# Kernel tuning notes

Measured on AMD Instinct MI355X. Metric: run time of the kernel, lower is better.

## Reference

```python
import jax, jax.numpy as jnp
import numpy as np
import math

B, K, T = 4, 1024, 2048
OD, H = 128, 8


def setup_inputs() -> dict:
    key = jax.random.key(0)
    ks = jax.random.split(key, 6)
    s_in = 1.0 / math.sqrt(K)
    s_u = 1.0 / math.sqrt(H * OD)
    return {
        "x": jax.random.normal(ks[0], (B, K, T), dtype=jnp.float32),
        "Wk": jax.random.uniform(ks[1], (H * OD, K), minval=-s_in, maxval=s_in, dtype=jnp.float32),
        "Wq": jax.random.uniform(ks[2], (H * OD, K), minval=-s_in, maxval=s_in, dtype=jnp.float32),
        "Wv": jax.random.uniform(ks[3], (H * OD, K), minval=-s_in, maxval=s_in, dtype=jnp.float32),
        "Wu": jax.random.uniform(ks[4], (OD, H * OD), minval=-s_u, maxval=s_u, dtype=jnp.float32),
        "bu": jax.random.uniform(ks[5], (OD,), minval=-s_u, maxval=s_u, dtype=jnp.float32),
    }


def reference(x, Wk, Wq, Wv, Wu, bu):
    b, k, t = x.shape
    # QKV projections: Linear applied over channel dim of channels-first input
    keys = jnp.einsum('bkt,jk->bjt', x, Wk).reshape(b, H, OD, t)
    queries = jnp.einsum('bkt,jk->bjt', x, Wq).reshape(b, H, OD, t)
    values = jnp.einsum('bkt,jk->bjt', x, Wv).reshape(b, H, OD, t)
    # attention scores over time: [b, h, t, t]
    dot = jnp.einsum('bhkt,bhki->bhti', queries, keys) / math.sqrt(OD)
    dot = jax.nn.softmax(dot, axis=-1)
    out = jnp.einsum('bhti,bhki->bhkt', dot, values)  # [b, h, od, t]
    # unify heads: weight (OD, H*OD) viewed as (OD_out=k, H=h, OD=e)
    out = jnp.einsum('bhet,khe->bkt', out, Wu.reshape(OD, H, OD))
    return out + bu[None, :, None]
```

## Files before the change

kernel.cpp:

```cpp
#include <hip/hip_runtime.h>
#include <hip/hip_bf16.h>
#include <type_traits>
#include <utility>

#define DEVINL __device__ __forceinline__

typedef unsigned short u16;
typedef unsigned int   u32;
typedef short  s8v  __attribute__((ext_vector_type(8)));
typedef __bf16 b8v  __attribute__((ext_vector_type(8)));
typedef float  f4v  __attribute__((ext_vector_type(4)));
typedef float  f16v __attribute__((ext_vector_type(16)));
typedef u32    u4v  __attribute__((ext_vector_type(4)));

static constexpr int BB = 4, KD = 1024, TT = 2048, OD = 128, NH = 8;
static constexpr int J2 = 2048;

template<class V, class = void> struct mfma_takes : std::false_type {};
template<class V> struct mfma_takes<V, std::void_t<decltype(
    __builtin_amdgcn_mfma_f32_16x16x32_bf16(std::declval<V>(), std::declval<V>(),
                                            std::declval<f4v>(), 0, 0, 0))>> : std::true_type {};

template<class AV>
DEVINL f4v mfma16(AV a, AV b, f4v c) {
  if constexpr (mfma_takes<AV>::value) {
    return __builtin_amdgcn_mfma_f32_16x16x32_bf16(a, b, c, 0, 0, 0);
  } else {
    return __builtin_amdgcn_mfma_f32_16x16x32_bf16(
        __builtin_bit_cast(b8v, a), __builtin_bit_cast(b8v, b), c, 0, 0, 0);
  }
}

template<class V, class = void> struct mfma32_takes : std::false_type {};
template<class V> struct mfma32_takes<V, std::void_t<decltype(
    __builtin_amdgcn_mfma_f32_32x32x16_bf16(std::declval<V>(), std::declval<V>(),
                                            std::declval<f16v>(), 0, 0, 0))>> : std::true_type {};

template<class AV>
DEVINL f16v mfma32(AV a, AV b, f16v c) {
  if constexpr (mfma32_takes<AV>::value) {
    return __builtin_amdgcn_mfma_f32_32x32x16_bf16(a, b, c, 0, 0, 0);
  } else {
    return __builtin_amdgcn_mfma_f32_32x32x16_bf16(
        __builtin_bit_cast(b8v, a), __builtin_bit_cast(b8v, b), c, 0, 0, 0);
  }
}

DEVINL u16 f2bf(float f) {
  union { float f; u32 u; } v; v.f = f;
  u32 u = v.u;
  return (u16)((u + 0x7fffu + ((u >> 16) & 1u)) >> 16);
}
DEVINL float bf2f(u16 h) { union { u32 u; float f; } v; v.u = ((u32)h) << 16; return v.f; }

DEVINL u32 cvtpk_bf16(float a, float b) {
  u32 r;
  asm("v_cvt_pk_bf16_f32 %0, %1, %2" : "=v"(r) : "v"(a), "v"(b));
  return r;
}

DEVINL void gload_lds16(const void* g, void* l) {
  __builtin_amdgcn_global_load_lds(
      (const __attribute__((address_space(1))) void*)g,
      (__attribute__((address_space(3))) void*)l, 16, 0, 0);
}

__global__ void xpose_split_x(const float* __restrict__ x, u16* __restrict__ xTh) {
  __shared__ float tile[32][33];
  const int b  = blockIdx.z;
  const int k0 = blockIdx.y * 32;
  const int t0 = blockIdx.x * 32;
  const int tx = threadIdx.x;
  const int ty = threadIdx.y;
  const float* xb = x + (size_t)b * KD * TT;
#pragma unroll
  for (int j = 0; j < 4; ++j)
    tile[ty + j * 8][tx] = xb[(size_t)(k0 + ty + j * 8) * TT + t0 + tx];
  __syncthreads();
  u16* oh = xTh + (size_t)b * TT * KD;
#pragma unroll
  for (int j = 0; j < 4; ++j) {
    int t = ty + j * 8;
    float v = tile[tx][t];
    oh[(size_t)(t0 + t) * KD + k0 + tx] = f2bf(v);
  }
}

__global__ void split_weights(const float* __restrict__ Wk, const float* __restrict__ Wq,
                              const float* __restrict__ Wv, const float* __restrict__ Wu,
                              u16* __restrict__ Wkqh, u16* __restrict__ Wvh,
                              u16* __restrict__ Wuh,  u16* __restrict__ Wul,
                              float qscale) {
  int i = blockIdx.x * 256 + threadIdx.x;
  if (i < 1048576) {
    Wkqh[i] = f2bf(Wk[i]);
    Wkqh[1048576 + i] = f2bf(Wq[i] * qscale);
    Wvh[i] = f2bf(Wv[i]);
    if (i < 131072) {
      float v = Wu[i];  u16 hh = f2bf(v);
      Wuh[i] = hh;      Wul[i] = f2bf(v - bf2f(hh));
    }
  }
}

template<int EPI>
__global__ __launch_bounds__(256, 3) void gemm_bt_split(
    const u16* __restrict__ Ahi, const u16* __restrict__ Alo,
    const u16* __restrict__ Bhi, const u16* __restrict__ Blo,
    void* __restrict__ Couth,
    const float* __restrict__ bias,
    int Kdim, int ldc, long strideA, long strideB, long strideC, int npass) {
  __shared__ __align__(16) u16 At[128 * 64];
  __shared__ __align__(16) u16 Bt[128 * 64];
  const int tid = threadIdx.x;
  const int w = tid >> 6, l = tid & 63;
  const int wm = w >> 1, wn = w & 1;
  const int lr = l & 15, lg = l >> 4;
  const int b = blockIdx.z;
  const u16* Ah = Ahi + (size_t)b * strideA;
  const u16* Al = Alo ? Alo + (size_t)b * strideA : nullptr;
  const u16* Bh = Bhi + (size_t)b * strideB;
  const u16* Bl = Blo ? Blo + (size_t)b * strideB : nullptr;
  const int m0 = blockIdx.x * 128;
  const int n0 = (EPI == 3) ? ((blockIdx.y & 15) * 128) : (blockIdx.y * 128);
  const int ky = (EPI == 3) ? (blockIdx.y >> 4) : 0;
  const int kspan = (EPI == 3) ? (Kdim / 2) : Kdim;
  const int kbase = ky * kspan;

  int srow[4], soff[4];
#pragma unroll
  for (int i = 0; i < 4; ++i) {
    int c = tid + i * 256;
    int row = c >> 3, q = c & 7;
    srow[i] = row;
    soff[i] = (q ^ (row & 7)) * 8;
  }

  f4v acc[4][4] = {};

  const int spi = kspan / 64;
  const int iters = npass * spi;
  for (int it = 0; it < iters; ++it) {
    const int seg = it / spi;
    const int k = kbase + (it - seg * spi) * 64;
    const u16* As = (seg == 2) ? Al : Ah;
    const u16* Bs = (seg == 1) ? Bl : Bh;
#pragma unroll
    for (int i = 0; i < 4; ++i) {
      int c = tid + i * 256;
      gload_lds16(As + (size_t)(m0 + srow[i]) * Kdim + k + soff[i], (char*)At + c * 16);
      gload_lds16(Bs + (size_t)(n0 + srow[i]) * Kdim + k + soff[i], (char*)Bt + c * 16);
    }
    __syncthreads();
    __builtin_amdgcn_s_setprio(1);
#pragma unroll
    for (int kk = 0; kk < 2; ++kk) {
      const int q = kk * 4 + lg;
      s8v a[4], bb[4];
#pragma unroll
      for (int mi = 0; mi < 4; ++mi) {
        int row = wm * 64 + mi * 16 + lr;
        a[mi] = *(const s8v*)(&At[row * 64 + (q ^ (row & 7)) * 8]);
      }
#pragma unroll
      for (int ni = 0; ni < 4; ++ni) {
        int row = wn * 64 + ni * 16 + lr;
        bb[ni] = *(const s8v*)(&Bt[row * 64 + (q ^ (row & 7)) * 8]);
      }
#pragma unroll
      for (int mi = 0; mi < 4; ++mi)
#pragma unroll
        for (int ni = 0; ni < 4; ++ni)
          acc[mi][ni] = mfma16(a[mi], bb[ni], acc[mi][ni]);
    }
    __builtin_amdgcn_s_setprio(0);
    __syncthreads();
  }

  if constexpr (EPI == 2) {
    u16* Ch = (u16*)Couth + (size_t)b * strideC;
#pragma unroll
    for (int mi = 0; mi < 4; ++mi)
#pragma unroll
      for (int ni = 0; ni < 4; ++ni)
#pragma unroll
        for (int r = 0; r < 4; ++r) {
          int m = m0 + wm * 64 + mi * 16 + lg * 4 + r;
          int n = n0 + wn * 64 + ni * 16 + lr;
          Ch[(size_t)m * ldc + n] = f2bf(acc[mi][ni][r]);
        }
  } else if constexpr (EPI == 3) {
    float* C = (float*)Couth + ((size_t)ky * BB + b) * strideC;
#pragma unroll
    for (int mi = 0; mi < 4; ++mi)
#pragma unroll
      for (int ni = 0; ni < 4; ++ni)
#pragma unroll
        for (int r = 0; r < 4; ++r) {
          int m = m0 + wm * 64 + mi * 16 + lg * 4 + r;
          int n = n0 + wn * 64 + ni * 16 + lr;
          C[(size_t)m * ldc + n] = acc[mi][ni][r];
        }
  } else {
    float* C = (float*)Couth + (size_t)b * strideC;
#pragma unroll
    for (int mi = 0; mi < 4; ++mi)
#pragma unroll
      for (int ni = 0; ni < 4; ++ni)
#pragma unroll
        for (int r = 0; r < 4; ++r) {
          int m = m0 + wm * 64 + mi * 16 + lg * 4 + r;
          int n = n0 + wn * 64 + ni * 16 + lr;
          C[(size_t)m * ldc + n] = acc[mi][ni][r] + bias[m];
        }
  }
}

__global__ void addbias(const float* __restrict__ part, float* __restrict__ out,
                        const float* __restrict__ bias) {
  int i = blockIdx.x * 256 + threadIdx.x;
  f4v a = ((const f4v*)part)[i];
  f4v c = ((const f4v*)part)[i + 262144];
  float bs = bias[(i >> 9) & 127];
  f4v r;
#pragma unroll
  for (int j = 0; j < 4; ++j) r[j] = a[j] + c[j] + bs;
  ((f4v*)out)[i] = r;
}

__global__ __launch_bounds__(256, 3) void attn_fwd(
    const u16* __restrict__ QKTh, const u16* __restrict__ Vh,
    u16* __restrict__ OTh, u16* __restrict__ OTl) {
  __shared__ __align__(16) u16 Ksh[2][32 * 128];
  __shared__ __align__(16) u16 Vsh[2][128 * 32];

  const int bid = blockIdx.x;
  const int lid = (bid & 7) * 64 + (bid >> 3);
  const int t0 = (lid & 15) * 128;
  const int h  = (lid >> 4) & 7;
  const int b  = lid >> 7;

  const int tid = threadIdx.x;
  const int w = tid >> 6, l = tid & 63;
  const int lw = l & 31, hi = l >> 5;
  const size_t qb = (size_t)b * TT * J2;
  const u16* Qh_ = QKTh + qb + 1024 + h * 128;
  const u16* Kh_ = QKTh + qb + h * 128;
  const u16* Vh_ = Vh + (size_t)b * 1024 * TT + (size_t)h * 128 * TT;

  int koff[2], kdo[2], voff[2], vdo[2];
#pragma unroll
  for (int i = 0; i < 2; ++i) {
    int c = tid + i * 256;
    { int row = c >> 4, q = c & 15;
      koff[i] = row * J2 + (q ^ (row & 7)) * 8;  kdo[i] = c * 16; }
    { int row = c >> 2, q = c & 3;
      voff[i] = row * TT + (q ^ ((row >> 1) & 3)) * 8;  vdo[i] = c * 16; }
  }

#define ATTN_STAGE(BSEL, I0) do {                                          \
    _Pragma("unroll")                                                      \
    for (int i_ = 0; i_ < 2; ++i_) {                                       \
      gload_lds16(Kh_ + (size_t)(I0) * J2 + koff[i_], (char*)Ksh[BSEL] + kdo[i_]); \
      gload_lds16(Vh_ + voff[i_] + (I0),              (char*)Vsh[BSEL] + vdo[i_]); \
    } } while (0)

  s8v qh[8];
  {
    const size_t trow = (size_t)(t0 + w * 32 + lw) * J2;
#pragma unroll
    for (int st = 0; st < 8; ++st)
      qh[st] = *(const s8v*)(Qh_ + trow + st * 16 + hi * 8);
  }

  f16v o[4] = {};
  float mrow = -1e30f, lsum = 0.f;

  ATTN_STAGE(0, 0);

  for (int it = 0; it < 64; ++it) {
    const int cur = it & 1;
    if (it + 1 < 64) {
      ATTN_STAGE(cur ^ 1, (it + 1) * 32);
      asm volatile("s_waitcnt vmcnt(4)" ::: "memory");
    } else {
      asm volatile("s_waitcnt vmcnt(0)" ::: "memory");
    }
    __builtin_amdgcn_s_barrier();

    const u16* Ks = Ksh[cur];
    const u16* Vs = Vsh[cur];
    f16v s = {};
    __builtin_amdgcn_s_setprio(1);
#pragma unroll
    for (int st = 0; st < 8; ++st) {
      s8v kf = *(const s8v*)(&Ks[lw * 128 + (((st * 2 + hi) ^ (lw & 7)) * 8)]);
      s = mfma32(kf, qh[st], s);
    }
    __builtin_amdgcn_s_setprio(0);

    float smax = s[0];
#pragma unroll
    for (int r = 1; r < 16; ++r) smax = fmaxf(smax, s[r]);
    smax = fmaxf(smax, __shfl_xor(smax, 32));

    if (__any(smax > mrow + 8.0f)) {
      float mn = fmaxf(mrow, smax);
      float al = exp2f(mrow - mn);
      mrow = mn;
      lsum *= al;
#pragma unroll
      for (int r = 0; r < 16; ++r) {
        float ar = __shfl(al, (r & 3) + 8 * (r >> 2) + 4 * hi);
#pragma unroll
        for (int et = 0; et < 4; ++et) o[et][r] *= ar;
      }
    }

    float rsum = 0.f;
#pragma unroll
    for (int r = 0; r < 16; ++r) { s[r] = exp2f(s[r] - mrow); rsum += s[r]; }
    rsum += __shfl_xor(rsum, 32);
    lsum += rsum;

    u32 wp[4][2];
#pragma unroll
    for (int g = 0; g < 4; ++g) {
      wp[g][0] = cvtpk_bf16(s[g * 4 + 0], s[g * 4 + 1]);
      wp[g][1] = cvtpk_bf16(s[g * 4 + 2], s[g * 4 + 3]);
    }
    s8v pa[2];
#pragma unroll
    for (int ks = 0; ks < 2; ++ks) {
      u32 a0 = wp[2 * ks][0], b0 = wp[2 * ks + 1][0];
      u32 a1 = wp[2 * ks][1], b1 = wp[2 * ks + 1][1];
      asm volatile("v_permlane32_swap_b32 %0, %1" : "+v"(a0), "+v"(b0));
      asm volatile("v_permlane32_swap_b32 %0, %1" : "+v"(a1), "+v"(b1));
      u4v fw; fw[0] = a0; fw[1] = a1; fw[2] = b0; fw[3] = b1;
      pa[ks] = __builtin_bit_cast(s8v, fw);
    }

    __builtin_amdgcn_s_setprio(1);
#pragma unroll
    for (int ks = 0; ks < 2; ++ks) {
#pragma unroll
      for (int et = 0; et < 4; ++et) {
        const int vrow = et * 32 + lw;
        s8v vh = *(const s8v*)(&Vs[vrow * 32 +
                                   (((ks * 2 + hi) ^ ((vrow >> 1) & 3)) * 8)]);
        o[et] = mfma32(pa[ks], vh, o[et]);
      }
    }
    __builtin_amdgcn_s_setprio(0);
    if (it + 1 < 64)
      __builtin_amdgcn_s_barrier();
  }
#undef ATTN_STAGE

  u16* oh = OTh + (size_t)b * TT * 1024;
  u16* ol = OTl + (size_t)b * TT * 1024;
#pragma unroll
  for (int r = 0; r < 16; ++r) {
    const int qrow = (r & 3) + 8 * (r >> 2) + 4 * hi;
    float ls = __shfl(lsum, qrow);
    float inv = 1.0f / ls;
    int t = t0 + w * 32 + qrow;
#pragma unroll
    for (int et = 0; et < 4; ++et) {
      int he = h * 128 + et * 32 + lw;
      float v = o[et][r] * inv;
      u16 hh = f2bf(v);
      oh[(size_t)t * 1024 + he] = hh;
      ol[(size_t)t * 1024 + he] = f2bf(v - bf2f(hh));
    }
  }
}

extern "C" void kernel_launch(void* const* d_in, const int* in_sizes, int n_in,
                              void* d_out, int out_size, void* d_ws, size_t ws_size,
                              hipStream_t stream) {
  const float* x  = (const float*)d_in[0];
  const float* Wk = (const float*)d_in[1];
  const float* Wq = (const float*)d_in[2];
  const float* Wv = (const float*)d_in[3];
  const float* Wu = (const float*)d_in[4];
  const float* bu = (const float*)d_in[5];
  float* out = (float*)d_out;

  const size_t need_bytes = 2ull * (8388608ull + 2097152ull + 1048576ull +
                                    131072ull * 2 + 16777216ull + 8388608ull +
                                    8388608ull * 2 + 4194304ull);
  if (ws_size < need_bytes) {
    hipMemsetAsync(d_out, 0, (size_t)out_size * sizeof(float), stream);
    return;
  }
  u16* p = (u16*)d_ws;
  u16* xTh = p;  p += 8388608;
  u16* Wkqh = p; p += 2097152;
  u16* Wvh = p;  p += 1048576;
  u16* Wuh = p;  p += 131072;
  u16* Wul = p;  p += 131072;
  u16* QKTh = p; p += 16777216;
  u16* Vh = p;   p += 8388608;
  u16* OTh = p;  p += 8388608;
  u16* OTl = p;  p += 8388608;
  float* Cpart = (float*)p; p += 4194304;

  const float qscale = 0.08838834764831845f * 1.4426950408889634f;

  xpose_split_x<<<dim3(64, 32, 4), dim3(32, 8), 0, stream>>>(x, xTh);
  split_weights<<<4096, 256, 0, stream>>>(Wk, Wq, Wv, Wu, Wkqh, Wvh, Wuh, Wul, qscale);

  gemm_bt_split<2><<<dim3(16, 16, 4), 256, 0, stream>>>(
      xTh, nullptr, Wkqh, nullptr, QKTh, nullptr,
      1024, 2048, 2097152L, 0L, 4194304L, 1);
  gemm_bt_split<2><<<dim3(8, 16, 4), 256, 0, stream>>>(
      Wvh, nullptr, xTh, nullptr, Vh, nullptr,
      1024, 2048, 0L, 2097152L, 2097152L, 1);
  attn_fwd<<<dim3(512), dim3(256), 0, stream>>>(QKTh, Vh, OTh, OTl);
  gemm_bt_split<3><<<dim3(1, 32, 4), 256, 0, stream>>>(
      Wuh, Wul, OTh, OTl, Cpart, nullptr,
      1024, 2048, 0L, 2097152L, 262144L, 3);
  addbias<<<1024, 256, 0, stream>>>(Cpart, out, bu);
}
```

Before: 201.0 us.

## Process two query tiles per wave in attention to reuse K/V LDS fragments

The attention kernel now runs with 128 threads (2 waves) per block instead of 4. Each wave handles 64 query rows as two 32-row sub-tiles, so every K and V fragment read from LDS feeds two MFMAs. Each thread issues twice as many global-to-LDS loads, and the wait count is adjusted to match. The aim is to cut LDS read traffic per MFMA and raise ILP. The cost is roughly double the accumulator and register footprint per wave, with fewer waves per block and a lower launch-bounds occupancy target.

New measurement: 336.8 us. 67.6% more time.

```diff
diff --git a/kernel.cpp b/kernel.cpp
--- a/kernel.cpp
+++ b/kernel.cpp
@@ -228,7 +228,7 @@
   ((f4v*)out)[i] = r;
 }
 
-__global__ __launch_bounds__(256, 3) void attn_fwd(
+__global__ __launch_bounds__(128, 2) void attn_fwd(
     const u16* __restrict__ QKTh, const u16* __restrict__ Vh,
     u16* __restrict__ OTh, u16* __restrict__ OTl) {
   __shared__ __align__(16) u16 Ksh[2][32 * 128];
@@ -248,10 +248,10 @@
   const u16* Kh_ = QKTh + qb + h * 128;
   const u16* Vh_ = Vh + (size_t)b * 1024 * TT + (size_t)h * 128 * TT;
 
-  int koff[2], kdo[2], voff[2], vdo[2];
-#pragma unroll
-  for (int i = 0; i < 2; ++i) {
-    int c = tid + i * 256;
+  int koff[4], kdo[4], voff[4], vdo[4];
+#pragma unroll
+  for (int i = 0; i < 4; ++i) {
+    int c = tid + i * 128;
     { int row = c >> 4, q = c & 15;
       koff[i] = row * J2 + (q ^ (row & 7)) * 8;  kdo[i] = c * 16; }
     { int row = c >> 2, q = c & 3;
@@ -260,21 +260,22 @@
 
 #define ATTN_STAGE(BSEL, I0) do {                                          \
     _Pragma("unroll")                                                      \
-    for (int i_ = 0; i_ < 2; ++i_) {                                       \
+    for (int i_ = 0; i_ < 4; ++i_) {                                       \
       gload_lds16(Kh_ + (size_t)(I0) * J2 + koff[i_], (char*)Ksh[BSEL] + kdo[i_]); \
       gload_lds16(Vh_ + voff[i_] + (I0),              (char*)Vsh[BSEL] + vdo[i_]); \
     } } while (0)
 
-  s8v qh[8];
-  {
-    const size_t trow = (size_t)(t0 + w * 32 + lw) * J2;
+  s8v qh[2][8];
+#pragma unroll
+  for (int j = 0; j < 2; ++j) {
+    const size_t trow = (size_t)(t0 + w * 64 + j * 32 + lw) * J2;
 #pragma unroll
     for (int st = 0; st < 8; ++st)
-      qh[st] = *(const s8v*)(Qh_ + trow + st * 16 + hi * 8);
-  }
-
-  f16v o[4] = {};
-  float mrow = -1e30f, lsum = 0.f;
+      qh[j][st] = *(const s8v*)(Qh_ + trow + st * 16 + hi * 8);
+  }
+
+  f16v o[2][4] = {};
+  float mrow[2] = {-1e30f, -1e30f}, lsum[2] = {0.f, 0.f};
 
   ATTN_STAGE(0, 0);
 
@@ -282,7 +283,7 @@
     const int cur = it & 1;
     if (it + 1 < 64) {
       ATTN_STAGE(cur ^ 1, (it + 1) * 32);
-      asm volatile("s_waitcnt vmcnt(4)" ::: "memory");
+      asm volatile("s_waitcnt vmcnt(8)" ::: "memory");
     } else {
       asm volatile("s_waitcnt vmcnt(0)" ::: "memory");
     }
@@ -290,54 +291,69 @@
 
     const u16* Ks = Ksh[cur];
     const u16* Vs = Vsh[cur];
-    f16v s = {};
+    f16v sA = {}, sB = {};
     __builtin_amdgcn_s_setprio(1);
 #pragma unroll
     for (int st = 0; st < 8; ++st) {
       s8v kf = *(const s8v*)(&Ks[lw * 128 + (((st * 2 + hi) ^ (lw & 7)) * 8)]);
-      s = mfma32(kf, qh[st], s);
+      sA = mfma32(kf, qh[0][st], sA);
+      sB = mfma32(kf, qh[1][st], sB);
     }
     __builtin_amdgcn_s_setprio(0);
 
-    float smax = s[0];
-#pragma unroll
-    for (int r = 1; r < 16; ++r) smax = fmaxf(smax, s[r]);
-    smax = fmaxf(smax, __shfl_xor(smax, 32));
-
-    if (__any(smax > mrow + 8.0f)) {
-      float mn = fmaxf(mrow, smax);
-      float al = exp2f(mrow - mn);
-      mrow = mn;
-      lsum *= al;
+    float smaxA = sA[0], smaxB = sB[0];
+#pragma unroll
+    for (int r = 1; r < 16; ++r) {
+      smaxA = fmaxf(smaxA, sA[r]);
+      smaxB = fmaxf(smaxB, sB[r]);
+    }
+    smaxA = fmaxf(smaxA, __shfl_xor(smaxA, 32));
+    smaxB = fmaxf(smaxB, __shfl_xor(smaxB, 32));
+
+    bool grow = (smaxA > mrow[0] + 8.0f) || (smaxB > mrow[1] + 8.0f);
+    if (__any(grow)) {
+      float mnA = fmaxf(mrow[0], smaxA), mnB = fmaxf(mrow[1], smaxB);
+      float alA = exp2f(mrow[0] - mnA), alB = exp2f(mrow[1] - mnB);
+      mrow[0] = mnA; mrow[1] = mnB;
+      lsum[0] *= alA; lsum[1] *= alB;
 #pragma unroll
       for (int r = 0; r < 16; ++r) {
-        float ar = __shfl(al, (r & 3) + 8 * (r >> 2) + 4 * hi);
-#pragma unroll
-        for (int et = 0; et < 4; ++et) o[et][r] *= ar;
-      }
-    }
-
-    float rsum = 0.f;
-#pragma unroll
-    for (int r = 0; r < 16; ++r) { s[r] = exp2f(s[r] - mrow); rsum += s[r]; }
-    rsum += __shfl_xor(rsum, 32);
-    lsum += rsum;
-
-    u32 wp[4][2];
-#pragma unroll
-    for (int g = 0; g < 4; ++g) {
-      wp[g][0] = cvtpk_bf16(s[g * 4 + 0], s[g * 4 + 1]);
-      wp[g][1] = cvtpk_bf16(s[g * 4 + 2], s[g * 4 + 3]);
-    }
-    s8v pa[2];
-#pragma unroll
-    for (int ks = 0; ks < 2; ++ks) {
-      u32 a0 = wp[2 * ks][0], b0 = wp[2 * ks + 1][0];
-      u32 a1 = wp[2 * ks][1], b1 = wp[2 * ks + 1][1];
-      asm volatile("v_permlane32_swap_b32 %0, %1" : "+v"(a0), "+v"(b0));
-      asm volatile("v_permlane32_swap_b32 %0, %1" : "+v"(a1), "+v"(b1));
-      u4v fw; fw[0] = a0; fw[1] = a1; fw[2] = b0; fw[3] = b1;
-      pa[ks] = __builtin_bit_cast(s8v, fw);
+        const int qrow = (r & 3) + 8 * (r >> 2) + 4 * hi;
+        float arA = __shfl(alA, qrow);
+        float arB = __shfl(alB, qrow);
+#pragma unroll
+        for (int et = 0; et < 4; ++et) { o[0][et][r] *= arA; o[1][et][r] *= arB; }
+      }
+    }
+
+    float rsA = 0.f, rsB = 0.f;
+#pragma unroll
+    for (int r = 0; r < 16; ++r) {
+      sA[r] = exp2f(sA[r] - mrow[0]); rsA += sA[r];
+      sB[r] = exp2f(sB[r] - mrow[1]); rsB += sB[r];
+    }
+    rsA += __shfl_xor(rsA, 32);  lsum[0] += rsA;
+    rsB += __shfl_xor(rsB, 32);  lsum[1] += rsB;
+
+    s8v pa[2][2];
+#pragma unroll
+    for (int j = 0; j < 2; ++j) {
+      f16v& s = j ? sB : sA;
+      u32 wp[4][2];
+#pragma unroll
+      for (int g = 0; g < 4; ++g) {
+        wp[g][0] = cvtpk_bf16(s[g * 4 + 0], s[g * 4 + 1]);
+        wp[g][1] = cvtpk_bf16(s[g * 4 + 2], s[g * 4 + 3]);
+      }
+#pragma unroll
+      for (int ks = 0; ks < 2; ++ks) {
+        u32 a0 = wp[2 * ks][0], b0 = wp[2 * ks + 1][0];
+        u32 a1 = wp[2 * ks][1], b1 = wp[2 * ks + 1][1];
+        asm volatile("v_permlane32_swap_b32 %0, %1" : "+v"(a0), "+v"(b0));
+        asm volatile("v_permlane32_swap_b32 %0, %1" : "+v"(a1), "+v"(b1));
+        u4v fw; fw[0] = a0; fw[1] = a1; fw[2] = b0; fw[3] = b1;
+        pa[j][ks] = __builtin_bit_cast(s8v, fw);
+      }
     }
 
     __builtin_amdgcn_s_setprio(1);
@@ -348,7 +364,8 @@
         const int vrow = et * 32 + lw;
         s8v vh = *(const s8v*)(&Vs[vrow * 32 +
                                    (((ks * 2 + hi) ^ ((vrow >> 1) & 3)) * 8)]);
-        o[et] = mfma32(pa[ks], vh, o[et]);
+        o[0][et] = mfma32(pa[0][ks], vh, o[0][et]);
+        o[1][et] = mfma32(pa[1][ks], vh, o[1][et]);
       }
     }
     __builtin_amdgcn_s_setprio(0);
@@ -360,20 +377,22 @@
   u16* oh = OTh + (size_t)b * TT * 1024;
   u16* ol = OTl + (size_t)b * TT * 1024;
 #pragma unroll
-  for (int r = 0; r < 16; ++r) {
-    const int qrow = (r & 3) + 8 * (r >> 2) + 4 * hi;
-    float ls = __shfl(lsum, qrow);
-    float inv = 1.0f / ls;
-    int t = t0 + w * 32 + qrow;
-#pragma unroll
-    for (int et = 0; et < 4; ++et) {
-      int he = h * 128 + et * 32 + lw;
-      float v = o[et][r] * inv;
-      u16 hh = f2bf(v);
-      oh[(size_t)t * 1024 + he] = hh;
-      ol[(size_t)t * 1024 + he] = f2bf(v - bf2f(hh));
-    }
-  }
+  for (int j = 0; j < 2; ++j)
+#pragma unroll
+    for (int r = 0; r < 16; ++r) {
+      const int qrow = (r & 3) + 8 * (r >> 2) + 4 * hi;
+      float ls = __shfl(lsum[j], qrow);
+      float inv = 1.0f / ls;
+      int t = t0 + w * 64 + j * 32 + qrow;
+#pragma unroll
+      for (int et = 0; et < 4; ++et) {
+        int he = h * 128 + et * 32 + lw;
+        float v = o[j][et][r] * inv;
+        u16 hh = f2bf(v);
+        oh[(size_t)t * 1024 + he] = hh;
+        ol[(size_t)t * 1024 + he] = f2bf(v - bf2f(hh));
+      }
+    }
 }
 
 extern "C" void kernel_launch(void* const* d_in, const int* in_sizes, int n_in,
@@ -417,7 +436,7 @@
   gemm_bt_split<2><<<dim3(8, 16, 4), 256, 0, stream>>>(
       Wvh, nullptr, xTh, nullptr, Vh, nullptr,
       1024, 2048, 0L, 2097152L, 2097152L, 1);
-  attn_fwd<<<dim3(512), dim3(256), 0, stream>>>(QKTh, Vh, OTh, OTl);
+  attn_fwd<<<dim3(512), dim3(128), 0, stream>>>(QKTh, Vh, OTh, OTl);
   gemm_bt_split<3><<<dim3(1, 32, 4), 256, 0, stream>>>(
       Wuh, Wul, OTh, OTl, Cpart, nullptr,
       1024, 2048, 0L, 2097152L, 262144L, 3);
```
